# Kernel tuning notes

Measured on AMD Instinct MI355X. Metric: run time of the kernel, lower is better.

Reference implementation:

```python
import jax, jax.numpy as jnp
import numpy as np

N, C, K, H = 131072, 256, 32, 8      # points, dim, patch_size, heads
NW = N // K                           # number of windows (4096)
POS_BND = int(0.8 * K)                # 25, as in OctFormer RPE (dilation=1)
RPE_NUM = 2 * POS_BND + 1             # 51


def layer_norm(x, g, b, eps=1e-5):
    m = x.mean(-1, keepdims=True)
    v = jnp.var(x, axis=-1, keepdims=True)
    return (x - m) * jax.lax.rsqrt(v + eps) * g + b


def setup_inputs() -> dict:
    key = jax.random.key(0)
    ks = jax.random.split(key, 12)
    s = 0.02
    return dict(
        data=jax.random.normal(ks[0], (N, C), jnp.float32),
        nbr_idx=jax.random.randint(ks[1], (N, 27), 0, N, dtype=jnp.int32),
        rel_pos=(jax.random.randint(ks[2], (NW, K, K, 3), 0, 2 * K + 1, dtype=jnp.int32) - K),
        patch_mask=jnp.zeros((NW, K, K), jnp.float32),
        w_cpe=jax.random.normal(ks[3], (27, C), jnp.float32) * s,
        bn_g=jnp.ones((C,), jnp.float32), bn_b=jnp.zeros((C,), jnp.float32),
        n1_g=jnp.ones((C,), jnp.float32), n1_b=jnp.zeros((C,), jnp.float32),
        w_qkv=jax.random.normal(ks[4], (C, 3 * C), jnp.float32) * s,
        b_qkv=jnp.zeros((3 * C,), jnp.float32),
        w_proj=jax.random.normal(ks[5], (C, C), jnp.float32) * s,
        b_proj=jnp.zeros((C,), jnp.float32),
        rpe_table=jax.random.normal(ks[6], (3 * RPE_NUM, H), jnp.float32) * s,
        n2_g=jnp.ones((C,), jnp.float32), n2_b=jnp.zeros((C,), jnp.float32),
        w_fc1=jax.random.normal(ks[7], (C, 4 * C), jnp.float32) * s,
        b_fc1=jnp.zeros((4 * C,), jnp.float32),
        w_fc2=jax.random.normal(ks[8], (4 * C, C), jnp.float32) * s,
        b_fc2=jnp.zeros((C,), jnp.float32),
    )


def reference(data, nbr_idx, rel_pos, patch_mask, w_cpe, bn_g, bn_b,
              n1_g, n1_b, w_qkv, b_qkv, w_proj, b_proj, rpe_table,
              n2_g, n2_b, w_fc1, b_fc1, w_fc2, b_fc2):
    # CPE: depthwise 27-neighbor octree conv + eval-mode batchnorm affine
    cpe = jnp.einsum('njc,jc->nc', data[nbr_idx], w_cpe)  # [N,27,C] gather
    data = data + (cpe * bn_g + bn_b)
    # data_to_windows: [N,C] -> [NW,K,C] (N divisible by K)
    x = data.reshape(NW, K, C)

    # windowed attention with inline RPE + additive patch mask
    h = layer_norm(x, n1_g, n1_b)
    qkv = (h @ w_qkv + b_qkv).reshape(NW, K, 3, H, C // H)
    q, k, v = qkv[:, :, 0], qkv[:, :, 1], qkv[:, :, 2]
    scale = (C // H) ** -0.5
    attn = jnp.einsum('nqhd,nkhd->nhqk', q * scale, k)     # [NW,H,K,K]
    idx = jnp.clip(rel_pos, -POS_BND, POS_BND) + POS_BND + jnp.arange(3) * RPE_NUM
    rpe = rpe_table[idx].sum(3)                             # [NW,K,K,H]
    attn = attn + rpe.transpose(0, 3, 1, 2) + patch_mask[:, None]
    attn = jax.nn.softmax(attn, axis=-1)
    out = jnp.einsum('nhqk,nkhd->nqhd', attn, v).reshape(NW, K, C)
    x = x + (out @ w_proj + b_proj)                         # gamma1 = 1

    # MLP (GELU, exact erf like torch default)
    h2 = layer_norm(x, n2_g, n2_b)
    x = x + (jax.nn.gelu(h2 @ w_fc1 + b_fc1, approximate=False) @ w_fc2 + b_fc2)
    return x.reshape(N, C)
```

## Files before the change

kernel.cpp:

```cpp
#include <hip/hip_runtime.h>
#include <stdint.h>


static constexpr int NPT   = 131072;
static constexpr int CC    = 256;
static constexpr int NWIN  = 4096;
static constexpr int NHEAD = 8;

using u16 = unsigned short;
using u32 = unsigned int;
using u8  = unsigned char;

typedef __bf16 bf16x8 __attribute__((ext_vector_type(8)));
typedef float  f32x4  __attribute__((ext_vector_type(4)));
typedef u32    u32x4  __attribute__((ext_vector_type(4)));
typedef u32    u32x2  __attribute__((ext_vector_type(2)));

__device__ __forceinline__ float b2f(u16 u) {
  union { float f; u32 i; } v; v.i = ((u32)u) << 16; return v.f;
}
__device__ __forceinline__ u16 f2b(float f) {
  u32 x = __float_as_uint(f);
  return (u16)((x + 0x7fffu + ((x >> 16) & 1u)) >> 16);
}

__device__ __forceinline__ u8 f2fp8(float f) {
  const u32 s = (__float_as_uint(f) >> 24) & 0x80u;
  float a = fabsf(f);
  if (a >= 0.015625f) {
    u32 b = __float_as_uint(a);
    u32 rb = b + 0x7FFFFu + ((b >> 20) & 1u);
    u32 E = (rb >> 23) - 120u;
    return (u8)(s | (E << 3) | ((rb >> 20) & 7u));
  }
  int k = (int)rintf(a * 512.0f);
  return (u8)(s | (u32)k);
}

template <int J>
__device__ __forceinline__ float fp82f(u32 d) {
#if defined(__has_builtin)
#if __has_builtin(__builtin_amdgcn_cvt_f32_fp8)
  return __builtin_amdgcn_cvt_f32_fp8(d, J);
#else
  const u32 u = (d >> (8 * J)) & 0xFFu;
  const u32 e = (u >> 3) & 15u, m = u & 7u;
  float v = e ? __uint_as_float(((e + 120u) << 23) | (m << 20))
              : (float)m * 0.001953125f;
  return (u & 0x80u) ? -v : v;
#endif
#else
  const u32 u = (d >> (8 * J)) & 0xFFu;
  const u32 e = (u >> 3) & 15u, m = u & 7u;
  float v = e ? __uint_as_float(((e + 120u) << 23) | (m << 20))
              : (float)m * 0.001953125f;
  return (u & 0x80u) ? -v : v;
#endif
}

__device__ __forceinline__ void gload_lds16(const void* g, void* l) {
  using gptr_t = const __attribute__((address_space(1))) uint32_t*;
  using lptr_t = __attribute__((address_space(3))) uint32_t*;
  __builtin_amdgcn_global_load_lds((gptr_t)(uintptr_t)g,
                                   (lptr_t)(uint32_t)(uintptr_t)l, 16, 0, 0);
}

__global__ __launch_bounds__(256) void k_f2b8(const float* __restrict__ in,
                                              u8* __restrict__ out, int n4) {
  for (int i = blockIdx.x * 256 + threadIdx.x; i < n4; i += gridDim.x * 256) {
    float4 v = ((const float4*)in)[i];
    u32 o = (u32)f2fp8(v.x) | ((u32)f2fp8(v.y) << 8) |
            ((u32)f2fp8(v.z) << 16) | ((u32)f2fp8(v.w) << 24);
    ((u32*)out)[i] = o;
  }
}

__global__ __launch_bounds__(256) void k_prep_w(
    const float* __restrict__ wqkv, const float* __restrict__ wproj,
    const float* __restrict__ wfc1, const float* __restrict__ wfc2,
    u16* __restrict__ oqkv, u16* __restrict__ oproj,
    u16* __restrict__ ofc1, u16* __restrict__ ofc2) {
  int i = blockIdx.x * 256 + threadIdx.x;
  if (i < 196608) {
    int c = i >> 8, r = i & 255; oqkv[i] = f2b(wqkv[r * 768 + c]);
  } else if (i < 262144) {
    i -= 196608; int c = i >> 8, r = i & 255; oproj[i] = f2b(wproj[r * 256 + c]);
  } else if (i < 524288) {
    i -= 262144; int c = i >> 8, r = i & 255; ofc1[i] = f2b(wfc1[r * 1024 + c]);
  } else {
    i -= 524288; int c = i >> 10, r = i & 1023; ofc2[i] = f2b(wfc2[r * 256 + c]);
  }
}

__global__ __launch_bounds__(256) void k_cpe_ln1(
    const float* __restrict__ data, const int* __restrict__ nbr,
    const u8* __restrict__ datab, const float* __restrict__ w_cpe,
    const float* __restrict__ bn_g, const float* __restrict__ bn_b,
    const float* __restrict__ n1_g, const float* __restrict__ n1_b,
    float* __restrict__ xo, u16* __restrict__ ho) {
  __shared__ __align__(16) u16 sW[27 * 256];
  const int tid = threadIdx.x;
  for (int i = tid; i < 864; i += 256) {
    float4 a = ((const float4*)w_cpe)[i * 2];
    float4 b = ((const float4*)w_cpe)[i * 2 + 1];
    u32x4 o;
    o[0] = (u32)f2b(a.x) | ((u32)f2b(a.y) << 16);
    o[1] = (u32)f2b(a.z) | ((u32)f2b(a.w) << 16);
    o[2] = (u32)f2b(b.x) | ((u32)f2b(b.y) << 16);
    o[3] = (u32)f2b(b.z) | ((u32)f2b(b.w) << 16);
    ((u32x4*)sW)[i] = o;
  }
  __syncthreads();

  const int wv   = tid >> 6;
  const int lane = tid & 63;
  const int c0   = lane * 4;
  const int n0   = blockIdx.x * 16 + wv * 4;

  const float4 g4  = *(const float4*)(bn_g + c0);
  const float4 b4  = *(const float4*)(bn_b + c0);
  const float4 ng  = *(const float4*)(n1_g + c0);
  const float4 nb4 = *(const float4*)(n1_b + c0);

#pragma unroll 1
  for (int p = 0; p < 4; p++) {
    const int n = n0 + p;
    int myidx = 0;
    if (lane < 27) myidx = nbr[n * 27 + lane];

    u32 d[27];
#pragma unroll
    for (int j = 0; j < 27; j++) {
      const int idx = __builtin_amdgcn_readlane(myidx, j);
      d[j] = *(const u32*)(datab + (size_t)idx * CC + c0);
    }

    float a0 = 0.f, a1 = 0.f, a2 = 0.f, a3 = 0.f;
#pragma unroll
    for (int j = 0; j < 27; j++) {
      const u32x2 wp = *(const u32x2*)&sW[j * 256 + c0];
      a0 += fp82f<0>(d[j]) * b2f((u16)(wp[0] & 0xffff));
      a1 += fp82f<1>(d[j]) * b2f((u16)(wp[0] >> 16));
      a2 += fp82f<2>(d[j]) * b2f((u16)(wp[1] & 0xffff));
      a3 += fp82f<3>(d[j]) * b2f((u16)(wp[1] >> 16));
    }

    const float4 dv = *(const float4*)(data + (size_t)n * CC + c0);
    float x0 = dv.x + a0 * g4.x + b4.x;
    float x1 = dv.y + a1 * g4.y + b4.y;
    float x2 = dv.z + a2 * g4.z + b4.z;
    float x3 = dv.w + a3 * g4.w + b4.w;
    *(float4*)(xo + (size_t)n * CC + c0) = make_float4(x0, x1, x2, x3);

    float s  = x0 + x1 + x2 + x3;
    float s2 = x0 * x0 + x1 * x1 + x2 * x2 + x3 * x3;
#pragma unroll
    for (int m = 1; m <= 32; m <<= 1) { s += __shfl_xor(s, m); s2 += __shfl_xor(s2, m); }
    const float mean = s * (1.f / 256.f);
    const float var  = s2 * (1.f / 256.f) - mean * mean;
    const float inv  = rsqrtf(var + 1e-5f);

    u32x2 o;
    o[0] = (u32)f2b((x0 - mean) * inv * ng.x + nb4.x) |
           ((u32)f2b((x1 - mean) * inv * ng.y + nb4.y) << 16);
    o[1] = (u32)f2b((x2 - mean) * inv * ng.z + nb4.z) |
           ((u32)f2b((x3 - mean) * inv * ng.w + nb4.w) << 16);
    *(u32x2*)(ho + (size_t)n * CC + c0) = o;
  }
}

template <int KD, int ND, int EPI>
__global__ __launch_bounds__(256) void k_gemm(const u16* __restrict__ A,
                                              const u16* __restrict__ Bt,
                                              const float* __restrict__ bias,
                                              u16* __restrict__ outb,
                                              float* __restrict__ outf) {
  constexpr int SMEM = (EPI == 1) ? 32768 : 34816;
  __shared__ __align__(16) char smem[SMEM];
  u16* As = (u16*)smem;
  u16* Bs = (u16*)(smem + 16384);
  const int tid = threadIdx.x;
  const int lane = tid & 63;
  const int wv = tid >> 6;
  const int wm = (wv >> 1) * 64;
  const int wn = (wv & 1) * 64;
  const int l15 = lane & 15;
  const int lhi = lane >> 4;

  const int gx = gridDim.x;
  const int bid = blockIdx.y * gx + blockIdx.x;
  const int cpx = (gx * gridDim.y) >> 3;
  const int swz = (bid & 7) * cpx + (bid >> 3);
  const int m0 = (swz / gx) * 128;
  const int n0 = (swz % gx) * 128;

  f32x4 acc[4][4] = {};

  for (int k0 = 0; k0 < KD; k0 += 64) {
#pragma unroll
    for (int i = 0; i < 4; i++) {
      const int off = i * 4096 + tid * 16;
      const int row = off >> 7;
      const int ke  = (off & 127) >> 1;
      gload_lds16(A  + (size_t)(m0 + row) * KD + k0 + ke, (char*)As + off);
      gload_lds16(Bt + (size_t)(n0 + row) * KD + k0 + ke, (char*)Bs + off);
    }
    __syncthreads();
#pragma unroll
    for (int kk = 0; kk < 2; kk++) {
      bf16x8 fa[4], fb[4];
#pragma unroll
      for (int t = 0; t < 4; t++) {
        fa[t] = *(const bf16x8*)&As[(wm + t * 16 + l15) * 64 + kk * 32 + lhi * 8];
        fb[t] = *(const bf16x8*)&Bs[(wn + t * 16 + l15) * 64 + kk * 32 + lhi * 8];
      }
#pragma unroll
      for (int mi = 0; mi < 4; mi++)
#pragma unroll
        for (int ni = 0; ni < 4; ni++)
          acc[mi][ni] = __builtin_amdgcn_mfma_f32_16x16x32_bf16(fa[mi], fb[ni],
                                                                acc[mi][ni], 0, 0, 0);
    }
    __syncthreads();
  }

  if constexpr (EPI == 1) {
#pragma unroll
    for (int mi = 0; mi < 4; mi++) {
#pragma unroll
      for (int ni = 0; ni < 4; ni++) {
        const int col = n0 + wn + ni * 16 + l15;
        const float bc = bias[col];
#pragma unroll
        for (int r = 0; r < 4; r++) {
          const int row = m0 + wm + mi * 16 + lhi * 4 + r;
          outf[(size_t)row * ND + col] += acc[mi][ni][r] + bc;
        }
      }
    }
  } else {
    u16* OL = (u16*)smem;
#pragma unroll
    for (int mi = 0; mi < 4; mi++) {
#pragma unroll
      for (int ni = 0; ni < 4; ni++) {
        const int lc = wn + ni * 16 + l15;
        const float bc = bias[n0 + lc];
#pragma unroll
        for (int r = 0; r < 4; r++) {
          float v = acc[mi][ni][r] + bc;
          if constexpr (EPI == 2)
            v = 0.5f * v * (1.0f + erff(v * 0.70710678118654752f));
          OL[(wm + mi * 16 + lhi * 4 + r) * 136 + lc] = f2b(v);
        }
      }
    }
    __syncthreads();
#pragma unroll
    for (int it = 0; it < 8; it++) {
      const int id = it * 256 + tid;
      const int row = id >> 4;
      const int cc = (id & 15) * 8;
      u32x4 w = *(const u32x4*)&OL[row * 136 + cc];
      *(u32x4*)(outb + (size_t)(m0 + row) * ND + n0 + cc) = w;
    }
  }
}

__global__ __launch_bounds__(256) void k_proj_ln2(
    const u16* __restrict__ A, const u16* __restrict__ Bt,
    const float* __restrict__ bias, float* __restrict__ xo,
    const float* __restrict__ n2g, const float* __restrict__ n2b,
    u16* __restrict__ h2) {
  __shared__ __align__(16) u16 As[128 * 64];
  __shared__ __align__(16) u16 Bs[256 * 64];
  const int tid = threadIdx.x;
  const int lane = tid & 63;
  const int wv = tid >> 6;
  const int l15 = lane & 15;
  const int g = lane >> 4;
  const int m0 = blockIdx.x * 128;
  const int wm = wv * 32;

  f32x4 acc[2][16] = {};

  for (int k0 = 0; k0 < 256; k0 += 64) {
#pragma unroll
    for (int i = 0; i < 4; i++) {
      const int off = i * 4096 + tid * 16;
      const int row = off >> 7, ke = (off & 127) >> 1;
      gload_lds16(A + (size_t)(m0 + row) * 256 + k0 + ke, (char*)As + off);
    }
#pragma unroll
    for (int i = 0; i < 8; i++) {
      const int off = i * 4096 + tid * 16;
      const int row = off >> 7, ke = (off & 127) >> 1;
      gload_lds16(Bt + (size_t)row * 256 + k0 + ke, (char*)Bs + off);
    }
    __syncthreads();
#pragma unroll
    for (int kk = 0; kk < 2; kk++) {
      bf16x8 fa[2];
#pragma unroll
      for (int t = 0; t < 2; t++)
        fa[t] = *(const bf16x8*)&As[(wm + t * 16 + l15) * 64 + kk * 32 + g * 8];
#pragma unroll
      for (int ni = 0; ni < 16; ni++) {
        bf16x8 fb = *(const bf16x8*)&Bs[(ni * 16 + l15) * 64 + kk * 32 + g * 8];
#pragma unroll
        for (int mi = 0; mi < 2; mi++)
          acc[mi][ni] = __builtin_amdgcn_mfma_f32_16x16x32_bf16(fa[mi], fb,
                                                                acc[mi][ni], 0, 0, 0);
      }
    }
    __syncthreads();
  }

#pragma unroll
  for (int mi = 0; mi < 2; mi++) {
#pragma unroll
    for (int r = 0; r < 4; r++) {
      const int row = m0 + wm + mi * 16 + g * 4 + r;
      float v[16];
      float s = 0.f, s2 = 0.f;
#pragma unroll
      for (int ni = 0; ni < 16; ni++) {
        const int col = ni * 16 + l15;
        float t = acc[mi][ni][r] + bias[col] + xo[(size_t)row * 256 + col];
        v[ni] = t; s += t; s2 += t * t;
      }
#pragma unroll
      for (int m = 1; m <= 8; m <<= 1) { s += __shfl_xor(s, m); s2 += __shfl_xor(s2, m); }
      const float mean = s * (1.f / 256.f);
      const float var  = s2 * (1.f / 256.f) - mean * mean;
      const float inv  = rsqrtf(var + 1e-5f);
#pragma unroll
      for (int ni = 0; ni < 16; ni++) {
        const int col = ni * 16 + l15;
        xo[(size_t)row * 256 + col] = v[ni];
        h2[(size_t)row * 256 + col] = f2b((v[ni] - mean) * inv * n2g[col] + n2b[col]);
      }
    }
  }
}

__global__ __launch_bounds__(512, 4) void k_attn(const u16* __restrict__ qkv,
                                                 const int* __restrict__ rel_pos,
                                                 const float* __restrict__ pmask,
                                                 const float* __restrict__ rpet,
                                                 u16* __restrict__ out) {
  constexpr int HS = 1288;
  __shared__ __align__(16) u16 smem[24 * HS + 2448];
  u16* sQ = smem;
  u16* sK = smem + 8 * HS;
  u16* sV = smem + 16 * HS;
  float* sT = (float*)(smem + 24 * HS);

  const int tid = threadIdx.x;
  const int nw  = blockIdx.x;
  const int w32 = nw * 32;

  for (int i = tid; i < 1224; i += 512) {
    int h = i / 153, ix = i - h * 153;
    sT[i] = rpet[ix * 8 + h];
  }
#pragma unroll
  for (int j = 0; j < 4; j++) {
    int id  = j * 512 + tid;
    int mat = id >> 10;
    int id1 = id & 1023;
    int h = id1 >> 7, q = (id1 >> 2) & 31, s = id1 & 3;
    u32x4 v = *(const u32x4*)(qkv + (size_t)(w32 + q) * 768 + mat * 256 + h * 32 + s * 8);
    u16* dst = (mat ? sK : sQ) + h * HS + q * 40 + s * 8;
    *(u32x4*)dst = v;
  }
#pragma unroll
  for (int j = 0; j < 2; j++) {
    int id = j * 512 + tid;
    int p = id >> 5, dc = id & 31;
    u32x4 v = *(const u32x4*)(qkv + (size_t)(w32 + p) * 768 + 512 + dc * 8);
    const u16* pv = (const u16*)&v;
#pragma unroll
    for (int jj = 0; jj < 8; jj++) {
      int d = dc * 8 + jj;
      sV[(d >> 5) * HS + (d & 31) * 40 + p] = pv[jj];
    }
  }
  __syncthreads();

  const int h = tid >> 6;
  const int lane = tid & 63;
  const int g = lane >> 4, c = lane & 15;
  const f32x4 zero = {0.f, 0.f, 0.f, 0.f};

  bf16x8 fq[2], fk[2];
#pragma unroll
  for (int t = 0; t < 2; t++) {
    fq[t] = *(const bf16x8*)&sQ[h * HS + (t * 16 + c) * 40 + g * 8];
    fk[t] = *(const bf16x8*)&sK[h * HS + (t * 16 + c) * 40 + g * 8];
  }
  f32x4 S[2][2];
#pragma unroll
  for (int qt = 0; qt < 2; qt++)
#pragma unroll
    for (int kt = 0; kt < 2; kt++)
      S[qt][kt] = __builtin_amdgcn_mfma_f32_16x16x32_bf16(fq[qt], fk[kt], zero, 0, 0, 0);

  const float sc = 0.17677669529663687f;
#pragma unroll
  for (int qt = 0; qt < 2; qt++) {
#pragma unroll
    for (int r = 0; r < 4; r++) {
      const int q = qt * 16 + g * 4 + r;
      const int* rp = rel_pos + ((size_t)(w32 + q) * 32) * 3;
      const float* pm = pmask + (size_t)(w32 + q) * 32;
      float v[2];
#pragma unroll
      for (int kt = 0; kt < 2; kt++) {
        const int k = kt * 16 + c;
        int r0 = rp[k * 3], r1 = rp[k * 3 + 1], r2 = rp[k * 3 + 2];
        r0 = min(max(r0, -25), 25);
        r1 = min(max(r1, -25), 25);
        r2 = min(max(r2, -25), 25);
        const float b = sT[h * 153 + 25 + r0] + sT[h * 153 + 76 + r1] +
                        sT[h * 153 + 127 + r2] + pm[k];
        v[kt] = S[qt][kt][r] * sc + b;
      }
      float m = fmaxf(v[0], v[1]);
#pragma unroll
      for (int d = 1; d <= 8; d <<= 1) m = fmaxf(m, __shfl_xor(m, d));
      const float e0 = __expf(v[0] - m);
      const float e1 = __expf(v[1] - m);
      float ssum = e0 + e1;
#pragma unroll
      for (int d = 1; d <= 8; d <<= 1) ssum += __shfl_xor(ssum, d);
      const float inv = 1.0f / ssum;
      sQ[h * HS + q * 40 + c]      = f2b(e0 * inv);
      sQ[h * HS + q * 40 + 16 + c] = f2b(e1 * inv);
    }
  }
  __builtin_amdgcn_sched_barrier(0);

  bf16x8 fp[2], fv[2];
#pragma unroll
  for (int t = 0; t < 2; t++) {
    fp[t] = *(const bf16x8*)&sQ[h * HS + (t * 16 + c) * 40 + g * 8];
    fv[t] = *(const bf16x8*)&sV[h * HS + (t * 16 + c) * 40 + g * 8];
  }
  f32x4 OT[2][2];
#pragma unroll
  for (int dt = 0; dt < 2; dt++)
#pragma unroll
    for (int qt = 0; qt < 2; qt++)
      OT[dt][qt] = __builtin_amdgcn_mfma_f32_16x16x32_bf16(fv[dt], fp[qt], zero, 0, 0, 0);

  __syncthreads();
  u16* OL = sK;
#pragma unroll
  for (int dt = 0; dt < 2; dt++)
#pragma unroll
    for (int qt = 0; qt < 2; qt++)
#pragma unroll
      for (int r = 0; r < 4; r++) {
        const int d = dt * 16 + g * 4 + r, q = qt * 16 + c;
        OL[q * 264 + h * 32 + d] = f2b(OT[dt][qt][r]);
      }
  __syncthreads();

  {
    const int q = tid >> 4, ch = tid & 15;
    u32x4 w0 = *(const u32x4*)&OL[q * 264 + ch * 16];
    u32x4 w1 = *(const u32x4*)&OL[q * 264 + ch * 16 + 8];
    u16* ob = out + (size_t)(w32 + q) * 256 + ch * 16;
    *(u32x4*)ob = w0;
    *((u32x4*)ob + 1) = w1;
  }
}

extern "C" void kernel_launch(void* const* d_in, const int* in_sizes, int n_in,
                              void* d_out, int out_size, void* d_ws, size_t ws_size,
                              hipStream_t stream) {
  const float* data   = (const float*)d_in[0];
  const int*   nbr    = (const int*)d_in[1];
  const int*   relpos = (const int*)d_in[2];
  const float* pmask  = (const float*)d_in[3];
  const float* w_cpe  = (const float*)d_in[4];
  const float* bn_g   = (const float*)d_in[5];
  const float* bn_b   = (const float*)d_in[6];
  const float* n1_g   = (const float*)d_in[7];
  const float* n1_b   = (const float*)d_in[8];
  const float* w_qkv  = (const float*)d_in[9];
  const float* b_qkv  = (const float*)d_in[10];
  const float* w_proj = (const float*)d_in[11];
  const float* b_proj = (const float*)d_in[12];
  const float* rpet   = (const float*)d_in[13];
  const float* n2_g   = (const float*)d_in[14];
  const float* n2_b   = (const float*)d_in[15];
  const float* w_fc1  = (const float*)d_in[16];
  const float* b_fc1  = (const float*)d_in[17];
  const float* w_fc2  = (const float*)d_in[18];
  const float* b_fc2  = (const float*)d_in[19];
  float* xout = (float*)d_out;

  char* pw = (char*)d_ws;
  u16* buf1 = (u16*)pw; pw += (size_t)NPT * 1024 * 2;
  u16* buf2 = (u16*)pw; pw += (size_t)NPT * 256 * 2;
  u16* wqkvT = (u16*)pw; pw += 768 * 256 * 2;
  u16* wprojT = (u16*)pw; pw += 256 * 256 * 2;
  u16* wfc1T = (u16*)pw; pw += 1024 * 256 * 2;
  u16* wfc2T = (u16*)pw; pw += 256 * 1024 * 2;
  u8* data8 = (u8*)buf1;

  k_f2b8<<<2048, 256, 0, stream>>>(data, data8, NPT * 256 / 4);
  k_prep_w<<<3072, 256, 0, stream>>>(w_qkv, w_proj, w_fc1, w_fc2,
                                     wqkvT, wprojT, wfc1T, wfc2T);

  k_cpe_ln1<<<NPT / 16, 256, 0, stream>>>(data, nbr, data8, w_cpe, bn_g, bn_b,
                                          n1_g, n1_b, xout, buf2);
  k_gemm<256, 768, 0><<<dim3(6, 1024), 256, 0, stream>>>(buf2, wqkvT, b_qkv, buf1, nullptr);
  k_attn<<<NWIN, 512, 0, stream>>>(buf1, relpos, pmask, rpet, buf2);
  k_proj_ln2<<<1024, 256, 0, stream>>>(buf2, wprojT, b_proj, xout, n2_g, n2_b, buf2);
  k_gemm<256, 1024, 2><<<dim3(8, 1024), 256, 0, stream>>>(buf2, wfc1T, b_fc1, buf1, nullptr);
  k_gemm<1024, 256, 1><<<dim3(2, 1024), 256, 0, stream>>>(buf1, wfc2T, b_fc2, nullptr, xout);
}
```

Before: 884.2 us.

## Fuse FC1+GELU and FC2 into one MLP kernel keeping hidden tile in LDS

Replaces the two separate MLP GEMM launches with a single k_ffn kernel. Each 128-row block computes the 1024-wide hidden activation in 128-column chunks, applies bias and GELU into LDS, and immediately accumulates the FC2 product in registers. This removes the write and re-read of the N×1024 bf16 intermediate in global memory. In exchange the kernel uses larger register accumulators, has limited in-block pipelining with many syncs, and launches only 1024 blocks.

```diff
diff --git a/kernel.cpp b/kernel.cpp
--- a/kernel.cpp
+++ b/kernel.cpp
@@ -169,14 +169,12 @@
   }
 }
 
-template <int KD, int ND, int EPI>
+template <int KD, int ND>
 __global__ __launch_bounds__(256) void k_gemm(const u16* __restrict__ A,
                                               const u16* __restrict__ Bt,
                                               const float* __restrict__ bias,
-                                              u16* __restrict__ outb,
-                                              float* __restrict__ outf) {
-  constexpr int SMEM = (EPI == 1) ? 32768 : 34816;
-  __shared__ __align__(16) char smem[SMEM];
+                                              u16* __restrict__ outb) {
+  __shared__ __align__(16) char smem[34816];
   u16* As = (u16*)smem;
   u16* Bs = (u16*)(smem + 16384);
   const int tid = threadIdx.x;
@@ -224,45 +222,133 @@
     __syncthreads();
   }
 
-  if constexpr (EPI == 1) {
-#pragma unroll
-    for (int mi = 0; mi < 4; mi++) {
-#pragma unroll
-      for (int ni = 0; ni < 4; ni++) {
-        const int col = n0 + wn + ni * 16 + l15;
-        const float bc = bias[col];
+  u16* OL = (u16*)smem;
+#pragma unroll
+  for (int mi = 0; mi < 4; mi++) {
+#pragma unroll
+    for (int ni = 0; ni < 4; ni++) {
+      const int lc = wn + ni * 16 + l15;
+      const float bc = bias[n0 + lc];
+#pragma unroll
+      for (int r = 0; r < 4; r++) {
+        OL[(wm + mi * 16 + lhi * 4 + r) * 136 + lc] = f2b(acc[mi][ni][r] + bc);
+      }
+    }
+  }
+  __syncthreads();
+#pragma unroll
+  for (int it = 0; it < 8; it++) {
+    const int id = it * 256 + tid;
+    const int row = id >> 4;
+    const int cc = (id & 15) * 8;
+    u32x4 w = *(const u32x4*)&OL[row * 136 + cc];
+    *(u32x4*)(outb + (size_t)(m0 + row) * ND + n0 + cc) = w;
+  }
+}
+
+__global__ __launch_bounds__(512) void k_ffn(
+    const u16* __restrict__ A,
+    const u16* __restrict__ W1,
+    const float* __restrict__ b1,
+    const u16* __restrict__ W2,
+    const float* __restrict__ b2,
+    float* __restrict__ xo) {
+  __shared__ __align__(16) char smem[32768 + 34816];
+  u16* As  = (u16*)smem;
+  u16* Bs  = (u16*)(smem + 16384);
+  u16* W2s = (u16*)smem;
+  u16* P   = (u16*)(smem + 32768);
+
+  const int tid = threadIdx.x;
+  const int lane = tid & 63;
+  const int wv = tid >> 6;
+  const int l15 = lane & 15;
+  const int lhi = lane >> 4;
+  const int m0 = blockIdx.x * 128;
+  const int wm = (wv >> 2) * 64;
+  const int wn = (wv & 3) * 32;
+
+  f32x4 acc2[16] = {};
+
+#pragma unroll 1
+  for (int nc = 0; nc < 8; nc++) {
+    f32x4 acc1[4][2] = {};
+    for (int k0 = 0; k0 < 256; k0 += 64) {
+#pragma unroll
+      for (int r = 0; r < 2; r++) {
+        const int off = r * 8192 + tid * 16;
+        const int row = off >> 7, ke = (off & 127) >> 1;
+        gload_lds16(A  + (size_t)(m0 + row) * 256 + k0 + ke, (char*)As + off);
+        gload_lds16(W1 + (size_t)(nc * 128 + row) * 256 + k0 + ke, (char*)Bs + off);
+      }
+      __syncthreads();
+#pragma unroll
+      for (int kk = 0; kk < 2; kk++) {
+        bf16x8 fa[4], fb[2];
+#pragma unroll
+        for (int t = 0; t < 4; t++)
+          fa[t] = *(const bf16x8*)&As[(wm + t * 16 + l15) * 64 + kk * 32 + lhi * 8];
+#pragma unroll
+        for (int u = 0; u < 2; u++)
+          fb[u] = *(const bf16x8*)&Bs[(wn + u * 16 + l15) * 64 + kk * 32 + lhi * 8];
+#pragma unroll
+        for (int t = 0; t < 4; t++)
+#pragma unroll
+          for (int u = 0; u < 2; u++)
+            acc1[t][u] = __builtin_amdgcn_mfma_f32_16x16x32_bf16(fa[t], fb[u],
+                                                                 acc1[t][u], 0, 0, 0);
+      }
+      __syncthreads();
+    }
+#pragma unroll
+    for (int t = 0; t < 4; t++) {
+#pragma unroll
+      for (int u = 0; u < 2; u++) {
+        const int col = wn + u * 16 + l15;
+        const float bc = b1[nc * 128 + col];
 #pragma unroll
         for (int r = 0; r < 4; r++) {
-          const int row = m0 + wm + mi * 16 + lhi * 4 + r;
-          outf[(size_t)row * ND + col] += acc[mi][ni][r] + bc;
+          float v = acc1[t][u][r] + bc;
+          v = 0.5f * v * (1.0f + erff(v * 0.70710678118654752f));
+          P[(wm + t * 16 + lhi * 4 + r) * 136 + col] = f2b(v);
         }
       }
     }
-  } else {
-    u16* OL = (u16*)smem;
-#pragma unroll
-    for (int mi = 0; mi < 4; mi++) {
-#pragma unroll
-      for (int ni = 0; ni < 4; ni++) {
-        const int lc = wn + ni * 16 + l15;
-        const float bc = bias[n0 + lc];
-#pragma unroll
-        for (int r = 0; r < 4; r++) {
-          float v = acc[mi][ni][r] + bc;
-          if constexpr (EPI == 2)
-            v = 0.5f * v * (1.0f + erff(v * 0.70710678118654752f));
-          OL[(wm + mi * 16 + lhi * 4 + r) * 136 + lc] = f2b(v);
+    __syncthreads();
+#pragma unroll 1
+    for (int kh = 0; kh < 2; kh++) {
+#pragma unroll
+      for (int r = 0; r < 4; r++) {
+        const int off = r * 8192 + tid * 16;
+        const int row = off >> 7, ke = (off & 127) >> 1;
+        gload_lds16(W2 + (size_t)row * 1024 + nc * 128 + kh * 64 + ke,
+                    (char*)W2s + off);
+      }
+      __syncthreads();
+#pragma unroll
+      for (int kks = 0; kks < 2; kks++) {
+        bf16x8 fa2 = *(const bf16x8*)&P[(wv * 16 + l15) * 136 +
+                                        kh * 64 + kks * 32 + lhi * 8];
+#pragma unroll
+        for (int ni = 0; ni < 16; ni++) {
+          bf16x8 fb2 = *(const bf16x8*)&W2s[(ni * 16 + l15) * 64 +
+                                            kks * 32 + lhi * 8];
+          acc2[ni] = __builtin_amdgcn_mfma_f32_16x16x32_bf16(fa2, fb2,
+                                                             acc2[ni], 0, 0, 0);
         }
       }
-    }
-    __syncthreads();
-#pragma unroll
-    for (int it = 0; it < 8; it++) {
-      const int id = it * 256 + tid;
-      const int row = id >> 4;
-      const int cc = (id & 15) * 8;
-      u32x4 w = *(const u32x4*)&OL[row * 136 + cc];
-      *(u32x4*)(outb + (size_t)(m0 + row) * ND + n0 + cc) = w;
+      __syncthreads();
+    }
+  }
+
+#pragma unroll
+  for (int ni = 0; ni < 16; ni++) {
+    const int col = ni * 16 + l15;
+    const float bc = b2[col];
+#pragma unroll
+    for (int r = 0; r < 4; r++) {
+      const int row = m0 + wv * 16 + lhi * 4 + r;
+      xo[(size_t)row * 256 + col] += acc2[ni][r] + bc;
     }
   }
 }
@@ -517,9 +603,8 @@
 
   k_cpe_ln1<<<NPT / 16, 256, 0, stream>>>(data, nbr, data8, w_cpe, bn_g, bn_b,
                                           n1_g, n1_b, xout, buf2);
-  k_gemm<256, 768, 0><<<dim3(6, 1024), 256, 0, stream>>>(buf2, wqkvT, b_qkv, buf1, nullptr);
+  k_gemm<256, 768><<<dim3(6, 1024), 256, 0, stream>>>(buf2, wqkvT, b_qkv, buf1);
   k_attn<<<NWIN, 512, 0, stream>>>(buf1, relpos, pmask, rpet, buf2);
   k_proj_ln2<<<1024, 256, 0, stream>>>(buf2, wprojT, b_proj, xout, n2_g, n2_b, buf2);
-  k_gemm<256, 1024, 2><<<dim3(8, 1024), 256, 0, stream>>>(buf2, wfc1T, b_fc1, buf1, nullptr);
-  k_gemm<1024, 256, 1><<<dim3(2, 1024), 256, 0, stream>>>(buf1, wfc2T, b_fc2, nullptr, xout);
-}
+  k_ffn<<<1024, 512, 0, stream>>>(buf2, wfc1T, b_fc1, wfc2T, b_fc2, xout);
+}
```

Result: slower. 1.011 ms (+14.3%).

## Fuse QKV projection GEMM into windowed attention kernel

Applied to the files above, without the earlier changes.

The separate QKV GEMM is removed. Each attention block now loads its 32-row LN1 tile into LDS and computes per-head Q, K and V with MFMA, reading weights directly from global memory, then runs attention from LDS. This avoids writing and re-reading the 131072x768 bf16 QKV intermediate and saves one kernel launch. In exchange, weight reuse is poor: every block streams the full 768x256 weight matrix through L2 without LDS tiling. The kernel also writes its output into the same buffer it reads its input from, and LDS use goes up.

```diff
diff --git a/kernel.cpp b/kernel.cpp
--- a/kernel.cpp
+++ b/kernel.cpp
@@ -344,60 +344,85 @@
   }
 }
 
-__global__ __launch_bounds__(512, 4) void k_attn(const u16* __restrict__ qkv,
-                                                 const int* __restrict__ rel_pos,
-                                                 const float* __restrict__ pmask,
-                                                 const float* __restrict__ rpet,
-                                                 u16* __restrict__ out) {
-  constexpr int HS = 1288;
-  __shared__ __align__(16) u16 smem[24 * HS + 2448];
-  u16* sQ = smem;
-  u16* sK = smem + 8 * HS;
-  u16* sV = smem + 16 * HS;
-  float* sT = (float*)(smem + 24 * HS);
+__global__ __launch_bounds__(512, 4) void k_attn(
+    const u16* __restrict__ hin, const u16* __restrict__ wqkv,
+    const float* __restrict__ bqkv, const int* __restrict__ rel_pos,
+    const float* __restrict__ pmask, const float* __restrict__ rpet,
+    u16* __restrict__ out) {
+  __shared__ __align__(16) u16 smem[38032];
+  u16* sH  = smem;
+  u16* sQ  = smem + 8448;
+  u16* sK  = smem + 16896;
+  u16* sVT = smem + 25344;
+  float* sT = (float*)(smem + 35584);
 
   const int tid = threadIdx.x;
   const int nw  = blockIdx.x;
   const int w32 = nw * 32;
-
-  for (int i = tid; i < 1224; i += 512) {
-    int h = i / 153, ix = i - h * 153;
-    sT[i] = rpet[ix * 8 + h];
-  }
-#pragma unroll
-  for (int j = 0; j < 4; j++) {
-    int id  = j * 512 + tid;
-    int mat = id >> 10;
-    int id1 = id & 1023;
-    int h = id1 >> 7, q = (id1 >> 2) & 31, s = id1 & 3;
-    u32x4 v = *(const u32x4*)(qkv + (size_t)(w32 + q) * 768 + mat * 256 + h * 32 + s * 8);
-    u16* dst = (mat ? sK : sQ) + h * HS + q * 40 + s * 8;
-    *(u32x4*)dst = v;
-  }
-#pragma unroll
-  for (int j = 0; j < 2; j++) {
-    int id = j * 512 + tid;
-    int p = id >> 5, dc = id & 31;
-    u32x4 v = *(const u32x4*)(qkv + (size_t)(w32 + p) * 768 + 512 + dc * 8);
-    const u16* pv = (const u16*)&v;
-#pragma unroll
-    for (int jj = 0; jj < 8; jj++) {
-      int d = dc * 8 + jj;
-      sV[(d >> 5) * HS + (d & 31) * 40 + p] = pv[jj];
-    }
-  }
-  __syncthreads();
-
   const int h = tid >> 6;
   const int lane = tid & 63;
   const int g = lane >> 4, c = lane & 15;
+
+  for (int i = tid; i < 1224; i += 512) {
+    int hh = i / 153, ix = i - hh * 153;
+    sT[i] = rpet[ix * 8 + hh];
+  }
+#pragma unroll
+  for (int it = 0; it < 2; it++) {
+    const int id = it * 512 + tid;
+    const int row = id >> 5, ch = (id & 31) * 8;
+    u32x4 v = *(const u32x4*)(hin + (size_t)(w32 + row) * 256 + ch);
+    *(u32x4*)&sH[row * 264 + ch] = v;
+  }
+  __syncthreads();
+
+  f32x4 aq[2][2] = {}, ak[2][2] = {}, av[2][2] = {};
+  const u16* wqb = wqkv + (size_t)(h * 32) * 256;
+  const u16* wkb = wqkv + (size_t)(256 + h * 32) * 256;
+  const u16* wvb = wqkv + (size_t)(512 + h * 32) * 256;
+#pragma unroll
+  for (int k0 = 0; k0 < 256; k0 += 32) {
+    bf16x8 fa[2];
+#pragma unroll
+    for (int t = 0; t < 2; t++)
+      fa[t] = *(const bf16x8*)&sH[(t * 16 + c) * 264 + k0 + g * 8];
+#pragma unroll
+    for (int u = 0; u < 2; u++) {
+      const size_t ro = (size_t)(u * 16 + c) * 256 + k0 + g * 8;
+      bf16x8 bq = *(const bf16x8*)(wqb + ro);
+      bf16x8 bk = *(const bf16x8*)(wkb + ro);
+      bf16x8 bv = *(const bf16x8*)(wvb + ro);
+#pragma unroll
+      for (int m = 0; m < 2; m++) {
+        aq[m][u] = __builtin_amdgcn_mfma_f32_16x16x32_bf16(fa[m], bq, aq[m][u], 0, 0, 0);
+        ak[m][u] = __builtin_amdgcn_mfma_f32_16x16x32_bf16(fa[m], bk, ak[m][u], 0, 0, 0);
+        av[m][u] = __builtin_amdgcn_mfma_f32_16x16x32_bf16(fa[m], bv, av[m][u], 0, 0, 0);
+      }
+    }
+  }
+#pragma unroll
+  for (int u = 0; u < 2; u++) {
+    const int d = u * 16 + c;
+    const float bq = bqkv[h * 32 + d];
+    const float bk = bqkv[256 + h * 32 + d];
+    const float bv = bqkv[512 + h * 32 + d];
+#pragma unroll
+    for (int m = 0; m < 2; m++)
+#pragma unroll
+      for (int r = 0; r < 4; r++) {
+        const int row = m * 16 + g * 4 + r;
+        sQ[row * 264 + h * 32 + d]   = f2b(aq[m][u][r] + bq);
+        sK[row * 264 + h * 32 + d]   = f2b(ak[m][u][r] + bk);
+        sVT[(h * 32 + d) * 40 + row] = f2b(av[m][u][r] + bv);
+      }
+  }
+
   const f32x4 zero = {0.f, 0.f, 0.f, 0.f};
-
   bf16x8 fq[2], fk[2];
 #pragma unroll
   for (int t = 0; t < 2; t++) {
-    fq[t] = *(const bf16x8*)&sQ[h * HS + (t * 16 + c) * 40 + g * 8];
-    fk[t] = *(const bf16x8*)&sK[h * HS + (t * 16 + c) * 40 + g * 8];
+    fq[t] = *(const bf16x8*)&sQ[(t * 16 + c) * 264 + h * 32 + g * 8];
+    fk[t] = *(const bf16x8*)&sK[(t * 16 + c) * 264 + h * 32 + g * 8];
   }
   f32x4 S[2][2];
 #pragma unroll
@@ -435,8 +460,8 @@
 #pragma unroll
       for (int d = 1; d <= 8; d <<= 1) ssum += __shfl_xor(ssum, d);
       const float inv = 1.0f / ssum;
-      sQ[h * HS + q * 40 + c]      = f2b(e0 * inv);
-      sQ[h * HS + q * 40 + 16 + c] = f2b(e1 * inv);
+      sQ[q * 264 + h * 32 + c]      = f2b(e0 * inv);
+      sQ[q * 264 + h * 32 + 16 + c] = f2b(e1 * inv);
     }
   }
   __builtin_amdgcn_sched_barrier(0);
@@ -444,8 +469,8 @@
   bf16x8 fp[2], fv[2];
 #pragma unroll
   for (int t = 0; t < 2; t++) {
-    fp[t] = *(const bf16x8*)&sQ[h * HS + (t * 16 + c) * 40 + g * 8];
-    fv[t] = *(const bf16x8*)&sV[h * HS + (t * 16 + c) * 40 + g * 8];
+    fp[t] = *(const bf16x8*)&sQ[(t * 16 + c) * 264 + h * 32 + g * 8];
+    fv[t] = *(const bf16x8*)&sVT[(h * 32 + t * 16 + c) * 40 + g * 8];
   }
   f32x4 OT[2][2];
 #pragma unroll
@@ -517,8 +542,7 @@
 
   k_cpe_ln1<<<NPT / 16, 256, 0, stream>>>(data, nbr, data8, w_cpe, bn_g, bn_b,
                                           n1_g, n1_b, xout, buf2);
-  k_gemm<256, 768, 0><<<dim3(6, 1024), 256, 0, stream>>>(buf2, wqkvT, b_qkv, buf1, nullptr);
-  k_attn<<<NWIN, 512, 0, stream>>>(buf1, relpos, pmask, rpet, buf2);
+  k_attn<<<NWIN, 512, 0, stream>>>(buf2, wqkvT, b_qkv, relpos, pmask, rpet, buf2);
   k_proj_ln2<<<1024, 256, 0, stream>>>(buf2, wprojT, b_proj, xout, n2_g, n2_b, buf2);
   k_gemm<256, 1024, 2><<<dim3(8, 1024), 256, 0, stream>>>(buf2, wfc1T, b_fc1, buf1, nullptr);
   k_gemm<1024, 256, 1><<<dim3(2, 1024), 256, 0, stream>>>(buf1, wfc2T, b_fc2, nullptr, xout);
```

New measurement: 906.2 us. 1.02x slower.
